# Kernel tuning notes

Measured on AMD Instinct MI355X. Metric: run time of the kernel, lower is better.

The kernel has to match this reference:

```python
import jax, jax.numpy as jnp
import numpy as np

D_MODEL = 768
N_HEADS = 12
D_K = D_MODEL // N_HEADS
EPS = 1e-5


def layer_norm(x, g, b):
    mu = jnp.mean(x, axis=-1, keepdims=True)
    var = jnp.var(x, axis=-1, keepdims=True)
    return (x - mu) * jax.lax.rsqrt(var + EPS) * g + b


def setup_inputs() -> dict:
    key = jax.random.key(0)
    ks = jax.random.split(key, 16)
    d, h = D_MODEL, 4 * D_MODEL
    s = 1.0 / np.sqrt(d)
    inp = {
        "x": jax.random.normal(ks[0], (2, 4096, d), jnp.float32),
        "wq": jax.random.normal(ks[1], (d, d), jnp.float32) * s,
        "bq": jnp.zeros((d,), jnp.float32),
        "wk": jax.random.normal(ks[2], (d, d), jnp.float32) * s,
        "bk": jnp.zeros((d,), jnp.float32),
        "wv": jax.random.normal(ks[3], (d, d), jnp.float32) * s,
        "bv": jnp.zeros((d,), jnp.float32),
        "wo": jax.random.normal(ks[4], (d, d), jnp.float32) * s,
        "bo": jnp.zeros((d,), jnp.float32),
        "w1": jax.random.normal(ks[5], (h, d), jnp.float32) * s,
        "b1": jnp.zeros((h,), jnp.float32),
        "w2": jax.random.normal(ks[6], (d, h), jnp.float32) * (1.0 / np.sqrt(h)),
        "b2": jnp.zeros((d,), jnp.float32),
        "g1": jnp.ones((d,), jnp.float32),
        "beta1": jnp.zeros((d,), jnp.float32),
        "g2": jnp.ones((d,), jnp.float32),
        "beta2": jnp.zeros((d,), jnp.float32),
    }
    return inp


def reference(x, wq, bq, wk, bk, wv, bv, wo, bo, w1, b1, w2, b2, g1, beta1, g2, beta2):
    B, S, D = x.shape
    # --- MHA (self-attention, torch Linear: y = x @ W.T + b) ---
    def heads(t):  # [B,S,D] -> [B,H,S,d_k]
        return t.reshape(B, S, N_HEADS, D_K).transpose(0, 2, 1, 3)
    q = heads(x @ wq.T + bq)
    k = heads(x @ wk.T + bk)
    v = heads(x @ wv.T + bv)
    scores = jnp.einsum("bhqd,bhkd->bhqk", q, k) / np.sqrt(D_K)
    attn = jax.nn.softmax(scores, axis=-1)
    ctx = jnp.einsum("bhqk,bhkd->bhqd", attn, v)
    ctx = ctx.transpose(0, 2, 1, 3).reshape(B, S, D)
    mha_out = ctx @ wo.T + bo
    # --- residual + LN1 ---
    n1 = layer_norm(x + mha_out, g1, beta1)
    # --- FFN (exact GELU, dropout=0/eval) ---
    hdn = jax.nn.gelu(n1 @ w1.T + b1, approximate=False)
    ffn_out = hdn @ w2.T + b2
    # --- residual + LN2 ---
    return layer_norm(n1 + ffn_out, g2, beta2)
```

## Files before the change

kernel.cpp:

```cpp
#include <hip/hip_runtime.h>
#include <cstdint>
#include <cstddef>


#define D_MODEL 768
#define N_HEADS 12
#define D_K     64
#define SEQ     4096
#define BATCH   2
#define M_ROWS  (BATCH * SEQ)
#define H_FF    3072
#define LDQKV   2304

#define QSCALE 0.18033688011112042f

typedef __bf16 bf16_t;
typedef __attribute__((ext_vector_type(8))) __bf16 bf16x8;
typedef __attribute__((ext_vector_type(4))) __bf16 bf16x4;
typedef __attribute__((ext_vector_type(2))) __bf16 bf16x2;
typedef __attribute__((ext_vector_type(4))) float  floatx4;
typedef __attribute__((ext_vector_type(4))) short  short4_t;

union bf16x4_cast { bf16x4 h; short4_t s; };

__device__ __forceinline__ float gelu_exact(float x) {
    return 0.5f * x * (1.0f + erff(x * 0.70710678118654752f));
}

#if __has_builtin(__builtin_amdgcn_exp2f)
#define EXP2F(x) __builtin_amdgcn_exp2f(x)
#else
static __device__ __forceinline__ float EXP2F(float x) {
    float r; asm("v_exp_f32 %0, %1" : "=v"(r) : "v"(x)); return r;
}
#endif

#define GLL16(gp, lp)                                                         \
    __builtin_amdgcn_global_load_lds(                                         \
        (const __attribute__((address_space(1))) void*)(gp),                  \
        (__attribute__((address_space(3))) void*)(lp), 16, 0, 0)

#define NX_V  (6291456 / 4)
#define NW_V  (589824 / 4)
#define NF_V  (2359296 / 4)
#define NCONV_V (NX_V + 4 * NW_V + 2 * NF_V)

__global__ __launch_bounds__(256) void fused_convert_kernel(
    const float* __restrict__ x,  const float* __restrict__ wq,
    const float* __restrict__ wk, const float* __restrict__ wv,
    const float* __restrict__ wo, const float* __restrict__ w1,
    const float* __restrict__ w2,
    bf16_t* __restrict__ xb, bf16_t* __restrict__ wqkvb,
    bf16_t* __restrict__ wob, bf16_t* __restrict__ w1b,
    bf16_t* __restrict__ w2b) {
    const int v = blockIdx.x * 256 + threadIdx.x;
    const float* src; bf16_t* dst; int off; float scale = 1.0f;
    if (v < NX_V)                    { src = x;  dst = xb;              off = v; }
    else if (v < NX_V + NW_V)        { src = wq; dst = wqkvb;           off = v - NX_V; scale = QSCALE; }
    else if (v < NX_V + 2 * NW_V)    { src = wk; dst = wqkvb + 589824;  off = v - NX_V - NW_V; }
    else if (v < NX_V + 3 * NW_V)    { src = wv; dst = wqkvb + 1179648; off = v - NX_V - 2 * NW_V; }
    else if (v < NX_V + 4 * NW_V)    { src = wo; dst = wob;             off = v - NX_V - 3 * NW_V; }
    else if (v < NX_V + 4 * NW_V + NF_V) { src = w1; dst = w1b;         off = v - NX_V - 4 * NW_V; }
    else                             { src = w2; dst = w2b;             off = v - NX_V - 4 * NW_V - NF_V; }
    floatx4 f = *(const floatx4*)&src[(size_t)off * 4];
    bf16x4 o = bf16x4{(bf16_t)(f[0] * scale), (bf16_t)(f[1] * scale),
                      (bf16_t)(f[2] * scale), (bf16_t)(f[3] * scale)};
    *(bf16x4*)&dst[(size_t)off * 4] = o;
}

__global__ __launch_bounds__(256) void pack_bias_kernel(
    const float* __restrict__ bq, const float* __restrict__ bk,
    const float* __restrict__ bv, float* __restrict__ dst) {
    int i = blockIdx.x * 256 + threadIdx.x;
    if (i < 768)       dst[i] = bq[i] * QSCALE;
    else if (i < 1536) dst[i] = bk[i - 768];
    else if (i < 2304) dst[i] = bv[i - 1536];
}

template<int BN>
__global__ __launch_bounds__(256) void gemm_lds_kernel(
    const bf16_t* __restrict__ A, const bf16_t* __restrict__ W,
    const float* __restrict__ bias, bf16_t* __restrict__ C,
    int M, int N, int K, int act) {

    __shared__ bf16_t As[128 * 64];
    __shared__ bf16_t Bs[BN * 64];

    const int t    = threadIdx.x;
    const int lane = t & 63;
    const int w    = t >> 6;
    const int lrow = lane & 15;
    const int quad = lane >> 4;
    const int n0   = blockIdx.x * BN;
    const int m0   = blockIdx.y * 128;

    constexpr int MI = (BN == 128) ? 4 : 2;
    constexpr int NB = (BN == 128) ? 4 : 2;
    const int wmo = (BN == 128) ? (w >> 1) * 64 : w * 32;
    const int wno = (BN == 128) ? (w & 1) * 64 : 0;

    const int srow = lane >> 3;
    const int scol = ((lane & 7) ^ srow) * 8;
    size_t a_g[4];
#pragma unroll
    for (int i = 0; i < 4; ++i)
        a_g[i] = (size_t)(m0 + (w * 4 + i) * 8 + srow) * K + scol;
    size_t b_g[NB];
#pragma unroll
    for (int i = 0; i < NB; ++i)
        b_g[i] = (size_t)(n0 + (w * NB + i) * 8 + srow) * K + scol;

    const int slot0 = (quad ^ (lrow & 7)) * 8;
    const int slot1 = slot0 ^ 32;

    floatx4 acc[MI][4];
#pragma unroll
    for (int i = 0; i < MI; ++i)
#pragma unroll
        for (int j = 0; j < 4; ++j) acc[i][j] = floatx4{0.f, 0.f, 0.f, 0.f};

    for (int k0 = 0; k0 < K; k0 += 64) {
#pragma unroll
        for (int i = 0; i < 4; ++i)
            GLL16(&A[a_g[i] + k0], &As[(w * 4 + i) * 512]);
#pragma unroll
        for (int i = 0; i < NB; ++i)
            GLL16(&W[b_g[i] + k0], &Bs[(w * NB + i) * 512]);
        __syncthreads();

#pragma unroll
        for (int kk = 0; kk < 2; ++kk) {
            const int off = kk ? slot1 : slot0;
            bf16x8 a[MI], b[4];
#pragma unroll
            for (int i = 0; i < MI; ++i)
                a[i] = *(bf16x8*)&As[(wmo + i * 16 + lrow) * 64 + off];
#pragma unroll
            for (int j = 0; j < 4; ++j)
                b[j] = *(bf16x8*)&Bs[(wno + j * 16 + lrow) * 64 + off];
#pragma unroll
            for (int i = 0; i < MI; ++i)
#pragma unroll
                for (int j = 0; j < 4; ++j)
                    acc[i][j] = __builtin_amdgcn_mfma_f32_16x16x32_bf16(
                        b[j], a[i], acc[i][j], 0, 0, 0);
        }
        __syncthreads();
    }

#pragma unroll
    for (int i = 0; i < MI; ++i) {
        const int m = m0 + wmo + i * 16 + lrow;
#pragma unroll
        for (int j = 0; j < 4; ++j) {
            const int n = n0 + wno + j * 16 + quad * 4;
            const floatx4 bv = *(const floatx4*)&bias[n];
            float v0 = acc[i][j][0] + bv[0];
            float v1 = acc[i][j][1] + bv[1];
            float v2 = acc[i][j][2] + bv[2];
            float v3 = acc[i][j][3] + bv[3];
            if (act) {
                v0 = gelu_exact(v0); v1 = gelu_exact(v1);
                v2 = gelu_exact(v2); v3 = gelu_exact(v3);
            }
            *(bf16x4*)&C[(size_t)m * N + n] =
                bf16x4{(bf16_t)v0, (bf16_t)v1, (bf16_t)v2, (bf16_t)v3};
        }
    }
}

__global__ __launch_bounds__(256, 3) void attn_kernel(
    const bf16_t* __restrict__ QKV, bf16_t* __restrict__ Ctx) {

    __shared__ bf16_t Ks[64 * 72];
    __shared__ bf16_t Vt[64 * 72];

    const int t    = threadIdx.x;
    const int lane = t & 63;
    const int w    = t >> 6;
    const int lrow = lane & 15;
    const int quad = lane >> 4;

    const int b  = blockIdx.y / N_HEADS;
    const int h  = blockIdx.y % N_HEADS;
    const int q0 = blockIdx.x * 128 + w * 32;
    const size_t base_q = ((size_t)b * SEQ) * LDQKV + h * D_K;
    const size_t base_k = base_q + 768;
    const size_t base_v = base_q + 1536;
    const size_t base_o = ((size_t)b * SEQ) * D_MODEL + h * D_K;

    bf16x8 qf[2][2];
#pragma unroll
    for (int s = 0; s < 2; ++s) {
        const size_t qrow = base_q + (size_t)(q0 + s * 16 + lrow) * LDQKV + quad * 8;
        qf[s][0] = *(const bf16x8*)&QKV[qrow];
        qf[s][1] = *(const bf16x8*)&QKV[qrow + 32];
    }

    float l_part[2] = {0.f, 0.f};
    floatx4 o_acc[2][4];
#pragma unroll
    for (int s = 0; s < 2; ++s)
#pragma unroll
        for (int d = 0; d < 4; ++d) o_acc[s][d] = floatx4{0.f, 0.f, 0.f, 0.f};

    const int skey = t >> 2;
    const int sch  = t & 3;
    const int kp   = t >> 3;
    const int sch8 = t & 7;
    const int vcol = ((2 * kp) & 63) ^ (sch8 << 3);

    const size_t gk0 = base_k + (size_t)skey * LDQKV + sch * 8;
    const size_t gv0 = base_v + (size_t)(2 * kp) * LDQKV + sch8 * 8;
    bf16x8 kv0 = *(const bf16x8*)&QKV[gk0];
    bf16x8 kv1 = *(const bf16x8*)&QKV[gk0 + 32];
    bf16x8 vv0 = *(const bf16x8*)&QKV[gv0];
    bf16x8 vv1 = *(const bf16x8*)&QKV[gv0 + LDQKV];

    for (int k0 = 0; k0 < SEQ; k0 += 64) {
        *(bf16x8*)&Ks[skey * 72 + sch * 8]      = kv0;
        *(bf16x8*)&Ks[skey * 72 + sch * 8 + 32] = kv1;
#pragma unroll
        for (int j = 0; j < 8; ++j)
            *(bf16x2*)&Vt[(sch8 * 8 + j) * 72 + vcol] = bf16x2{vv0[j], vv1[j]};
        __syncthreads();

        if (k0 + 64 < SEQ) {
            const size_t gk = gk0 + (size_t)(k0 + 64) * LDQKV;
            const size_t gv = gv0 + (size_t)(k0 + 64) * LDQKV;
            kv0 = *(const bf16x8*)&QKV[gk];
            kv1 = *(const bf16x8*)&QKV[gk + 32];
            vv0 = *(const bf16x8*)&QKV[gv];
            vv1 = *(const bf16x8*)&QKV[gv + LDQKV];
        }

        __builtin_amdgcn_s_setprio(1);
        short4_t p[2][4];
#pragma unroll
        for (int kt = 0; kt < 4; ++kt) {
            bf16x8 ka0 = *(bf16x8*)&Ks[(kt * 16 + lrow) * 72 + quad * 8];
            bf16x8 ka1 = *(bf16x8*)&Ks[(kt * 16 + lrow) * 72 + 32 + quad * 8];
            floatx4 z = floatx4{0.f, 0.f, 0.f, 0.f};
#pragma unroll
            for (int s = 0; s < 2; ++s) {
                floatx4 st = __builtin_amdgcn_mfma_f32_16x16x32_bf16(ka0, qf[s][0], z, 0, 0, 0);
                st = __builtin_amdgcn_mfma_f32_16x16x32_bf16(ka1, qf[s][1], st, 0, 0, 0);
                float p0 = EXP2F(st[0]), p1 = EXP2F(st[1]);
                float p2 = EXP2F(st[2]), p3 = EXP2F(st[3]);
                l_part[s] += (p0 + p1) + (p2 + p3);
                bf16x4_cast pc;
                pc.h = bf16x4{(bf16_t)p0, (bf16_t)p1, (bf16_t)p2, (bf16_t)p3};
                p[s][kt] = pc.s;
            }
        }

#pragma unroll
        for (int dt = 0; dt < 4; ++dt) {
            const int d   = dt * 16 + lrow;
            const int swv = ((d >> 3) & 7) << 3;
#pragma unroll
            for (int kc = 0; kc < 4; ++kc) {
                bf16x4_cast ac;
                ac.h = *(bf16x4*)&Vt[d * 72 + ((kc * 16 + quad * 4) ^ swv)];
                o_acc[0][dt] = __builtin_amdgcn_mfma_f32_16x16x16bf16_1k(
                    ac.s, p[0][kc], o_acc[0][dt], 0, 0, 0);
                o_acc[1][dt] = __builtin_amdgcn_mfma_f32_16x16x16bf16_1k(
                    ac.s, p[1][kc], o_acc[1][dt], 0, 0, 0);
            }
        }
        __builtin_amdgcn_s_setprio(0);
        __syncthreads();
    }

#pragma unroll
    for (int s = 0; s < 2; ++s) {
        float lsum = l_part[s];
        lsum += __shfl_xor(lsum, 16, 64);
        lsum += __shfl_xor(lsum, 32, 64);
        const float inv = 1.0f / lsum;
        const size_t orow = base_o + (size_t)(q0 + s * 16 + lrow) * D_MODEL;
#pragma unroll
        for (int dt = 0; dt < 4; ++dt) {
            bf16x4 ov = bf16x4{(bf16_t)(o_acc[s][dt][0] * inv),
                               (bf16_t)(o_acc[s][dt][1] * inv),
                               (bf16_t)(o_acc[s][dt][2] * inv),
                               (bf16_t)(o_acc[s][dt][3] * inv)};
            *(bf16x4*)&Ctx[orow + dt * 16 + quad * 4] = ov;
        }
    }
}

__global__ __launch_bounds__(256) void ln_res_f32in_kernel(
    const float* __restrict__ x, const bf16_t* __restrict__ res,
    const float* __restrict__ g, const float* __restrict__ be,
    bf16_t* __restrict__ out) {
    const int row = blockIdx.x, t = threadIdx.x;
    const size_t base = (size_t)row * D_MODEL;
    float vals[3], sum = 0.f, sq = 0.f;
#pragma unroll
    for (int it = 0; it < 3; ++it) {
        int i = t + it * 256;
        float v = x[base + i] + (float)res[base + i];
        vals[it] = v; sum += v; sq += v * v;
    }
#pragma unroll
    for (int d = 1; d < 64; d <<= 1) { sum += __shfl_xor(sum, d, 64); sq += __shfl_xor(sq, d, 64); }
    __shared__ float ssum[4], ssq[4], s_mu, s_rs;
    if ((t & 63) == 0) { ssum[t >> 6] = sum; ssq[t >> 6] = sq; }
    __syncthreads();
    if (t == 0) {
        float S = ssum[0] + ssum[1] + ssum[2] + ssum[3];
        float Qq = ssq[0] + ssq[1] + ssq[2] + ssq[3];
        float mu = S / D_MODEL;
        s_mu = mu;
        s_rs = rsqrtf(Qq / D_MODEL - mu * mu + 1e-5f);
    }
    __syncthreads();
    const float mu = s_mu, rs = s_rs;
#pragma unroll
    for (int it = 0; it < 3; ++it) {
        int i = t + it * 256;
        out[base + i] = (bf16_t)((vals[it] - mu) * rs * g[i] + be[i]);
    }
}

__global__ __launch_bounds__(256) void ln_res_final_kernel(
    const bf16_t* __restrict__ a, const bf16_t* __restrict__ bfb,
    const float* __restrict__ g, const float* __restrict__ be,
    float* __restrict__ out) {
    const int row = blockIdx.x, t = threadIdx.x;
    const size_t base = (size_t)row * D_MODEL;
    float vals[3], sum = 0.f, sq = 0.f;
#pragma unroll
    for (int it = 0; it < 3; ++it) {
        int i = t + it * 256;
        float v = (float)a[base + i] + (float)bfb[base + i];
        vals[it] = v; sum += v; sq += v * v;
    }
#pragma unroll
    for (int d = 1; d < 64; d <<= 1) { sum += __shfl_xor(sum, d, 64); sq += __shfl_xor(sq, d, 64); }
    __shared__ float ssum[4], ssq[4], s_mu, s_rs;
    if ((t & 63) == 0) { ssum[t >> 6] = sum; ssq[t >> 6] = sq; }
    __syncthreads();
    if (t == 0) {
        float S = ssum[0] + ssum[1] + ssum[2] + ssum[3];
        float Qq = ssq[0] + ssq[1] + ssq[2] + ssq[3];
        float mu = S / D_MODEL;
        s_mu = mu;
        s_rs = rsqrtf(Qq / D_MODEL - mu * mu + 1e-5f);
    }
    __syncthreads();
    const float mu = s_mu, rs = s_rs;
#pragma unroll
    for (int it = 0; it < 3; ++it) {
        int i = t + it * 256;
        out[base + i] = (vals[it] - mu) * rs * g[i] + be[i];
    }
}

extern "C" void kernel_launch(void* const* d_in, const int* in_sizes, int n_in,
                              void* d_out, int out_size, void* d_ws, size_t ws_size,
                              hipStream_t stream) {
    const float* x    = (const float*)d_in[0];
    const float* wq   = (const float*)d_in[1];
    const float* bq   = (const float*)d_in[2];
    const float* wk   = (const float*)d_in[3];
    const float* bk   = (const float*)d_in[4];
    const float* wv   = (const float*)d_in[5];
    const float* bv   = (const float*)d_in[6];
    const float* wo   = (const float*)d_in[7];
    const float* bo   = (const float*)d_in[8];
    const float* w1   = (const float*)d_in[9];
    const float* b1   = (const float*)d_in[10];
    const float* w2   = (const float*)d_in[11];
    const float* b2   = (const float*)d_in[12];
    const float* g1   = (const float*)d_in[13];
    const float* be1  = (const float*)d_in[14];
    const float* g2   = (const float*)d_in[15];
    const float* be2  = (const float*)d_in[16];
    float* out = (float*)d_out;

    char* ws = (char*)d_ws;
    const size_t SZ_XB   = (size_t)M_ROWS * D_MODEL * 2;
    const size_t SZ_QKV  = (size_t)M_ROWS * LDQKV * 2;
    const size_t SZ_CTX  = SZ_XB;
    const size_t SZ_H    = (size_t)M_ROWS * H_FF * 2;
    const size_t SZ_WQKV = (size_t)LDQKV * D_MODEL * 2;
    const size_t SZ_WO   = (size_t)D_MODEL * D_MODEL * 2;
    const size_t SZ_W1   = (size_t)H_FF * D_MODEL * 2;

    bf16_t* xb    = (bf16_t*)(ws);
    bf16_t* qkvb  = (bf16_t*)(ws + SZ_XB);
    bf16_t* ctxb  = (bf16_t*)(ws + SZ_XB + SZ_QKV);
    bf16_t* hb    = (bf16_t*)(ws + SZ_XB + SZ_QKV + SZ_CTX);
    char*   wsw   = ws + SZ_XB + SZ_QKV + SZ_CTX + SZ_H;
    bf16_t* wqkvb = (bf16_t*)(wsw);
    bf16_t* wob   = (bf16_t*)(wsw + SZ_WQKV);
    bf16_t* w1b   = (bf16_t*)(wsw + SZ_WQKV + SZ_WO);
    bf16_t* w2b   = (bf16_t*)(wsw + SZ_WQKV + SZ_WO + SZ_W1);
    float*  bqkv  = (float*)(wsw + SZ_WQKV + SZ_WO + 2 * SZ_W1);
    bf16_t* mhab  = qkvb;
    bf16_t* n1b   = xb;
    bf16_t* ffb   = ctxb;

    fused_convert_kernel<<<NCONV_V / 256, 256, 0, stream>>>(
        x, wq, wk, wv, wo, w1, w2, xb, wqkvb, wob, w1b, w2b);
    pack_bias_kernel<<<9, 256, 0, stream>>>(bq, bk, bv, bqkv);

    gemm_lds_kernel<128><<<dim3(LDQKV / 128, M_ROWS / 128), 256, 0, stream>>>(
        xb, wqkvb, bqkv, qkvb, M_ROWS, LDQKV, D_MODEL, 0);

    attn_kernel<<<dim3(SEQ / 128, BATCH * N_HEADS), 256, 0, stream>>>(qkvb, ctxb);

    gemm_lds_kernel<64><<<dim3(D_MODEL / 64, M_ROWS / 128), 256, 0, stream>>>(
        ctxb, wob, bo, mhab, M_ROWS, D_MODEL, D_MODEL, 0);

    ln_res_f32in_kernel<<<M_ROWS, 256, 0, stream>>>(x, mhab, g1, be1, n1b);

    gemm_lds_kernel<128><<<dim3(H_FF / 128, M_ROWS / 128), 256, 0, stream>>>(
        n1b, w1b, b1, hb, M_ROWS, H_FF, D_MODEL, 1);

    gemm_lds_kernel<64><<<dim3(D_MODEL / 64, M_ROWS / 128), 256, 0, stream>>>(
        hb, w2b, b2, ffb, M_ROWS, D_MODEL, H_FF, 0);

    ln_res_final_kernel<<<M_ROWS, 256, 0, stream>>>(n1b, ffb, g2, be2, out);
}
```

Baseline: 483.0 us.

## Split-K the FFN down-projection and fold partial sums into final LayerNorm

Replaces the W2 GEMM (K=3072, N=768, 64-wide tiles) with a 128x128-tile split-K kernel whose two halves write fp32 partials into the output buffer and the reused QKV buffer. The final residual LayerNorm kernel now sums both partials and adds the bias itself. The aim is larger tiles with better data reuse while keeping enough blocks in flight, and no bf16 rounding of the FFN output. In exchange, the fp32 partials add extra global memory writes and reads.

```diff
diff --git a/kernel.cpp b/kernel.cpp
--- a/kernel.cpp
+++ b/kernel.cpp
@@ -169,6 +169,85 @@
     }
 }
 
+__global__ __launch_bounds__(256) void gemm_splitk_kernel(
+    const bf16_t* __restrict__ A, const bf16_t* __restrict__ W,
+    float* __restrict__ P0, float* __restrict__ P1,
+    int M, int N, int K) {
+
+    __shared__ bf16_t As[128 * 64];
+    __shared__ bf16_t Bs[128 * 64];
+
+    const int t    = threadIdx.x;
+    const int lane = t & 63;
+    const int w    = t >> 6;
+    const int lrow = lane & 15;
+    const int quad = lane >> 4;
+    const int n0   = blockIdx.x * 128;
+    const int m0   = blockIdx.y * 128;
+    const int kb   = blockIdx.z * (K / 2);
+
+    const int wmo = (w >> 1) * 64;
+    const int wno = (w & 1) * 64;
+
+    const int srow = lane >> 3;
+    const int scol = ((lane & 7) ^ srow) * 8;
+    size_t a_g[4], b_g[4];
+#pragma unroll
+    for (int i = 0; i < 4; ++i) {
+        a_g[i] = (size_t)(m0 + (w * 4 + i) * 8 + srow) * K + kb + scol;
+        b_g[i] = (size_t)(n0 + (w * 4 + i) * 8 + srow) * K + kb + scol;
+    }
+
+    const int slot0 = (quad ^ (lrow & 7)) * 8;
+    const int slot1 = slot0 ^ 32;
+
+    floatx4 acc[4][4];
+#pragma unroll
+    for (int i = 0; i < 4; ++i)
+#pragma unroll
+        for (int j = 0; j < 4; ++j) acc[i][j] = floatx4{0.f, 0.f, 0.f, 0.f};
+
+    for (int k0 = 0; k0 < K / 2; k0 += 64) {
+#pragma unroll
+        for (int i = 0; i < 4; ++i)
+            GLL16(&A[a_g[i] + k0], &As[(w * 4 + i) * 512]);
+#pragma unroll
+        for (int i = 0; i < 4; ++i)
+            GLL16(&W[b_g[i] + k0], &Bs[(w * 4 + i) * 512]);
+        __syncthreads();
+
+#pragma unroll
+        for (int kk = 0; kk < 2; ++kk) {
+            const int off = kk ? slot1 : slot0;
+            bf16x8 a[4], b[4];
+#pragma unroll
+            for (int i = 0; i < 4; ++i)
+                a[i] = *(bf16x8*)&As[(wmo + i * 16 + lrow) * 64 + off];
+#pragma unroll
+            for (int j = 0; j < 4; ++j)
+                b[j] = *(bf16x8*)&Bs[(wno + j * 16 + lrow) * 64 + off];
+#pragma unroll
+            for (int i = 0; i < 4; ++i)
+#pragma unroll
+                for (int j = 0; j < 4; ++j)
+                    acc[i][j] = __builtin_amdgcn_mfma_f32_16x16x32_bf16(
+                        b[j], a[i], acc[i][j], 0, 0, 0);
+        }
+        __syncthreads();
+    }
+
+    float* __restrict__ P = blockIdx.z ? P1 : P0;
+#pragma unroll
+    for (int i = 0; i < 4; ++i) {
+        const int m = m0 + wmo + i * 16 + lrow;
+#pragma unroll
+        for (int j = 0; j < 4; ++j) {
+            const int n = n0 + wno + j * 16 + quad * 4;
+            *(floatx4*)&P[(size_t)m * N + n] = acc[i][j];
+        }
+    }
+}
+
 __global__ __launch_bounds__(256, 3) void attn_kernel(
     const bf16_t* __restrict__ QKV, bf16_t* __restrict__ Ctx) {
 
@@ -325,7 +404,8 @@
 }
 
 __global__ __launch_bounds__(256) void ln_res_final_kernel(
-    const bf16_t* __restrict__ a, const bf16_t* __restrict__ bfb,
+    const bf16_t* __restrict__ a, const float* __restrict__ p0,
+    const float* __restrict__ p1, const float* __restrict__ b2,
     const float* __restrict__ g, const float* __restrict__ be,
     float* __restrict__ out) {
     const int row = blockIdx.x, t = threadIdx.x;
@@ -334,7 +414,7 @@
 #pragma unroll
     for (int it = 0; it < 3; ++it) {
         int i = t + it * 256;
-        float v = (float)a[base + i] + (float)bfb[base + i];
+        float v = (float)a[base + i] + p0[base + i] + p1[base + i] + b2[i];
         vals[it] = v; sum += v; sq += v * v;
     }
 #pragma unroll
@@ -401,7 +481,8 @@
     float*  bqkv  = (float*)(wsw + SZ_WQKV + SZ_WO + 2 * SZ_W1);
     bf16_t* mhab  = qkvb;
     bf16_t* n1b   = xb;
-    bf16_t* ffb   = ctxb;
+    float*  p0    = out;
+    float*  p1    = (float*)qkvb;
 
     fused_convert_kernel<<<NCONV_V / 256, 256, 0, stream>>>(
         x, wq, wk, wv, wo, w1, w2, xb, wqkvb, wob, w1b, w2b);
@@ -420,8 +501,8 @@
     gemm_lds_kernel<128><<<dim3(H_FF / 128, M_ROWS / 128), 256, 0, stream>>>(
         n1b, w1b, b1, hb, M_ROWS, H_FF, D_MODEL, 1);
 
-    gemm_lds_kernel<64><<<dim3(D_MODEL / 64, M_ROWS / 128), 256, 0, stream>>>(
-        hb, w2b, b2, ffb, M_ROWS, D_MODEL, H_FF, 0);
-
-    ln_res_final_kernel<<<M_ROWS, 256, 0, stream>>>(n1b, ffb, g2, be2, out);
-}
+    gemm_splitk_kernel<<<dim3(D_MODEL / 128, M_ROWS / 128, 2), 256, 0, stream>>>(
+        hb, w2b, p0, p1, M_ROWS, D_MODEL, H_FF);
+
+    ln_res_final_kernel<<<M_ROWS, 256, 0, stream>>>(n1b, p0, p1, b2, g2, be2, out);
+}
```

Result: no change. 486.9 us (+0.8%).

## Double-buffer K/V shared tiles in attention kernel to drop one barrier per tile

Applied to the files above, without the earlier changes.

Attention now keeps two shared-memory buffers for the K and transposed V tiles. Each iteration computes on the current buffer, then writes the already-prefetched next tile into the other buffer and issues global loads two tiles ahead. This removes one __syncthreads per key tile and lets the LDS writes overlap with other waves' compute. In exchange it doubles LDS use (about 36KB per block), which may lower occupancy under the 3-blocks-per-SM launch bound, and the register-prefetched global loads must now complete before the store at the end of the same iteration.

```diff
diff --git a/kernel.cpp b/kernel.cpp
--- a/kernel.cpp
+++ b/kernel.cpp
@@ -172,8 +172,8 @@
 __global__ __launch_bounds__(256, 3) void attn_kernel(
     const bf16_t* __restrict__ QKV, bf16_t* __restrict__ Ctx) {
 
-    __shared__ bf16_t Ks[64 * 72];
-    __shared__ bf16_t Vt[64 * 72];
+    __shared__ bf16_t Ks[2][64 * 72];
+    __shared__ bf16_t Vt[2][64 * 72];
 
     const int t    = threadIdx.x;
     const int lane = t & 63;
@@ -212,34 +212,37 @@
 
     const size_t gk0 = base_k + (size_t)skey * LDQKV + sch * 8;
     const size_t gv0 = base_v + (size_t)(2 * kp) * LDQKV + sch8 * 8;
+
     bf16x8 kv0 = *(const bf16x8*)&QKV[gk0];
     bf16x8 kv1 = *(const bf16x8*)&QKV[gk0 + 32];
     bf16x8 vv0 = *(const bf16x8*)&QKV[gv0];
     bf16x8 vv1 = *(const bf16x8*)&QKV[gv0 + LDQKV];
-
+    *(bf16x8*)&Ks[0][skey * 72 + sch * 8]      = kv0;
+    *(bf16x8*)&Ks[0][skey * 72 + sch * 8 + 32] = kv1;
+#pragma unroll
+    for (int j = 0; j < 8; ++j)
+        *(bf16x2*)&Vt[0][(sch8 * 8 + j) * 72 + vcol] = bf16x2{vv0[j], vv1[j]};
+    {
+        const size_t gk = gk0 + (size_t)64 * LDQKV;
+        const size_t gv = gv0 + (size_t)64 * LDQKV;
+        kv0 = *(const bf16x8*)&QKV[gk];
+        kv1 = *(const bf16x8*)&QKV[gk + 32];
+        vv0 = *(const bf16x8*)&QKV[gv];
+        vv1 = *(const bf16x8*)&QKV[gv + LDQKV];
+    }
+    __syncthreads();
+
+    int cur = 0;
     for (int k0 = 0; k0 < SEQ; k0 += 64) {
-        *(bf16x8*)&Ks[skey * 72 + sch * 8]      = kv0;
-        *(bf16x8*)&Ks[skey * 72 + sch * 8 + 32] = kv1;
-#pragma unroll
-        for (int j = 0; j < 8; ++j)
-            *(bf16x2*)&Vt[(sch8 * 8 + j) * 72 + vcol] = bf16x2{vv0[j], vv1[j]};
-        __syncthreads();
-
-        if (k0 + 64 < SEQ) {
-            const size_t gk = gk0 + (size_t)(k0 + 64) * LDQKV;
-            const size_t gv = gv0 + (size_t)(k0 + 64) * LDQKV;
-            kv0 = *(const bf16x8*)&QKV[gk];
-            kv1 = *(const bf16x8*)&QKV[gk + 32];
-            vv0 = *(const bf16x8*)&QKV[gv];
-            vv1 = *(const bf16x8*)&QKV[gv + LDQKV];
-        }
+        const bf16_t* ks = Ks[cur];
+        const bf16_t* vt = Vt[cur];
 
         __builtin_amdgcn_s_setprio(1);
         short4_t p[2][4];
 #pragma unroll
         for (int kt = 0; kt < 4; ++kt) {
-            bf16x8 ka0 = *(bf16x8*)&Ks[(kt * 16 + lrow) * 72 + quad * 8];
-            bf16x8 ka1 = *(bf16x8*)&Ks[(kt * 16 + lrow) * 72 + 32 + quad * 8];
+            bf16x8 ka0 = *(bf16x8*)&ks[(kt * 16 + lrow) * 72 + quad * 8];
+            bf16x8 ka1 = *(bf16x8*)&ks[(kt * 16 + lrow) * 72 + 32 + quad * 8];
             floatx4 z = floatx4{0.f, 0.f, 0.f, 0.f};
 #pragma unroll
             for (int s = 0; s < 2; ++s) {
@@ -261,7 +264,7 @@
 #pragma unroll
             for (int kc = 0; kc < 4; ++kc) {
                 bf16x4_cast ac;
-                ac.h = *(bf16x4*)&Vt[d * 72 + ((kc * 16 + quad * 4) ^ swv)];
+                ac.h = *(bf16x4*)&vt[d * 72 + ((kc * 16 + quad * 4) ^ swv)];
                 o_acc[0][dt] = __builtin_amdgcn_mfma_f32_16x16x16bf16_1k(
                     ac.s, p[0][kc], o_acc[0][dt], 0, 0, 0);
                 o_acc[1][dt] = __builtin_amdgcn_mfma_f32_16x16x16bf16_1k(
@@ -269,7 +272,26 @@
             }
         }
         __builtin_amdgcn_s_setprio(0);
+
+        if (k0 + 64 < SEQ) {
+            bf16_t* ksn = Ks[cur ^ 1];
+            bf16_t* vtn = Vt[cur ^ 1];
+            *(bf16x8*)&ksn[skey * 72 + sch * 8]      = kv0;
+            *(bf16x8*)&ksn[skey * 72 + sch * 8 + 32] = kv1;
+#pragma unroll
+            for (int j = 0; j < 8; ++j)
+                *(bf16x2*)&vtn[(sch8 * 8 + j) * 72 + vcol] = bf16x2{vv0[j], vv1[j]};
+            if (k0 + 128 < SEQ) {
+                const size_t gk = gk0 + (size_t)(k0 + 128) * LDQKV;
+                const size_t gv = gv0 + (size_t)(k0 + 128) * LDQKV;
+                kv0 = *(const bf16x8*)&QKV[gk];
+                kv1 = *(const bf16x8*)&QKV[gk + 32];
+                vv0 = *(const bf16x8*)&QKV[gv];
+                vv1 = *(const bf16x8*)&QKV[gv + LDQKV];
+            }
+        }
         __syncthreads();
+        cur ^= 1;
     }
 
 #pragma unroll
```

Result: no change. 490.8 us (+1.6%).

## Double-buffer K/V shared memory tiles in attention kernel

Applied to the files above, without the earlier changes.

Splits the K and V shared-memory tiles into two buffers and unrolls the key loop by two. While one tile is being computed, the next tile is written to the other buffer, so there is one barrier per tile instead of two. This is meant to overlap LDS writes and global prefetch with the MFMA work and cut synchronisation stalls. The cost is double the LDS footprint and extra registers for two prefetched tiles, which could reduce occupancy.

```diff
diff --git a/kernel.cpp b/kernel.cpp
--- a/kernel.cpp
+++ b/kernel.cpp
@@ -172,8 +172,8 @@
 __global__ __launch_bounds__(256, 3) void attn_kernel(
     const bf16_t* __restrict__ QKV, bf16_t* __restrict__ Ctx) {
 
-    __shared__ bf16_t Ks[64 * 72];
-    __shared__ bf16_t Vt[64 * 72];
+    __shared__ bf16_t Ks[2][64 * 72];
+    __shared__ bf16_t Vt[2][64 * 72];
 
     const int t    = threadIdx.x;
     const int lane = t & 63;
@@ -212,63 +212,84 @@
 
     const size_t gk0 = base_k + (size_t)skey * LDQKV + sch * 8;
     const size_t gv0 = base_v + (size_t)(2 * kp) * LDQKV + sch8 * 8;
-    bf16x8 kv0 = *(const bf16x8*)&QKV[gk0];
-    bf16x8 kv1 = *(const bf16x8*)&QKV[gk0 + 32];
-    bf16x8 vv0 = *(const bf16x8*)&QKV[gv0];
-    bf16x8 vv1 = *(const bf16x8*)&QKV[gv0 + LDQKV];
-
-    for (int k0 = 0; k0 < SEQ; k0 += 64) {
-        *(bf16x8*)&Ks[skey * 72 + sch * 8]      = kv0;
-        *(bf16x8*)&Ks[skey * 72 + sch * 8 + 32] = kv1;
-#pragma unroll
-        for (int j = 0; j < 8; ++j)
-            *(bf16x2*)&Vt[(sch8 * 8 + j) * 72 + vcol] = bf16x2{vv0[j], vv1[j]};
+
+#define ATTN_LOAD(koff, KV0, KV1, VV0, VV1)                                   \
+    {                                                                         \
+        const size_t gk_ = gk0 + (size_t)(koff) * LDQKV;                      \
+        const size_t gv_ = gv0 + (size_t)(koff) * LDQKV;                      \
+        KV0 = *(const bf16x8*)&QKV[gk_];                                      \
+        KV1 = *(const bf16x8*)&QKV[gk_ + 32];                                 \
+        VV0 = *(const bf16x8*)&QKV[gv_];                                      \
+        VV1 = *(const bf16x8*)&QKV[gv_ + LDQKV];                              \
+    }
+
+#define ATTN_WRITE(BUF, KV0, KV1, VV0, VV1)                                   \
+    {                                                                         \
+        bf16_t* ksn_ = Ks[BUF];                                               \
+        bf16_t* vtn_ = Vt[BUF];                                               \
+        *(bf16x8*)&ksn_[skey * 72 + sch * 8]      = KV0;                      \
+        *(bf16x8*)&ksn_[skey * 72 + sch * 8 + 32] = KV1;                      \
+        _Pragma("unroll")                                                     \
+        for (int j = 0; j < 8; ++j)                                           \
+            *(bf16x2*)&vtn_[(sch8 * 8 + j) * 72 + vcol] = bf16x2{VV0[j], VV1[j]}; \
+    }
+
+#define ATTN_COMPUTE(CUR)                                                     \
+    {                                                                         \
+        const bf16_t* ks_ = Ks[CUR];                                          \
+        const bf16_t* vt_ = Vt[CUR];                                          \
+        __builtin_amdgcn_s_setprio(1);                                        \
+        short4_t p[2][4];                                                     \
+        _Pragma("unroll")                                                     \
+        for (int kt = 0; kt < 4; ++kt) {                                      \
+            bf16x8 ka0 = *(bf16x8*)&ks_[(kt * 16 + lrow) * 72 + quad * 8];    \
+            bf16x8 ka1 = *(bf16x8*)&ks_[(kt * 16 + lrow) * 72 + 32 + quad * 8]; \
+            floatx4 z = floatx4{0.f, 0.f, 0.f, 0.f};                          \
+            _Pragma("unroll")                                                 \
+            for (int s = 0; s < 2; ++s) {                                     \
+                floatx4 st = __builtin_amdgcn_mfma_f32_16x16x32_bf16(ka0, qf[s][0], z, 0, 0, 0); \
+                st = __builtin_amdgcn_mfma_f32_16x16x32_bf16(ka1, qf[s][1], st, 0, 0, 0); \
+                float p0 = EXP2F(st[0]), p1 = EXP2F(st[1]);                   \
+                float p2 = EXP2F(st[2]), p3 = EXP2F(st[3]);                   \
+                l_part[s] += (p0 + p1) + (p2 + p3);                           \
+                bf16x4_cast pc;                                               \
+                pc.h = bf16x4{(bf16_t)p0, (bf16_t)p1, (bf16_t)p2, (bf16_t)p3}; \
+                p[s][kt] = pc.s;                                              \
+            }                                                                 \
+        }                                                                     \
+        _Pragma("unroll")                                                     \
+        for (int dt = 0; dt < 4; ++dt) {                                      \
+            const int d_  = dt * 16 + lrow;                                   \
+            const int swv = ((d_ >> 3) & 7) << 3;                             \
+            _Pragma("unroll")                                                 \
+            for (int kc = 0; kc < 4; ++kc) {                                  \
+                bf16x4_cast ac;                                               \
+                ac.h = *(bf16x4*)&vt_[d_ * 72 + ((kc * 16 + quad * 4) ^ swv)]; \
+                o_acc[0][dt] = __builtin_amdgcn_mfma_f32_16x16x16bf16_1k(     \
+                    ac.s, p[0][kc], o_acc[0][dt], 0, 0, 0);                   \
+                o_acc[1][dt] = __builtin_amdgcn_mfma_f32_16x16x16bf16_1k(     \
+                    ac.s, p[1][kc], o_acc[1][dt], 0, 0, 0);                   \
+            }                                                                 \
+        }                                                                     \
+        __builtin_amdgcn_s_setprio(0);                                        \
+    }
+
+    bf16x8 akv0, akv1, avv0, avv1;
+    bf16x8 bkv0, bkv1, bvv0, bvv1;
+
+    ATTN_LOAD(0, akv0, akv1, avv0, avv1);
+    ATTN_WRITE(0, akv0, akv1, avv0, avv1);
+    ATTN_LOAD(64, bkv0, bkv1, bvv0, bvv1);
+    __syncthreads();
+
+    for (int k0 = 0; k0 < SEQ; k0 += 128) {
+        if (k0 + 128 < SEQ) ATTN_LOAD(k0 + 128, akv0, akv1, avv0, avv1);
+        ATTN_COMPUTE(0);
+        ATTN_WRITE(1, bkv0, bkv1, bvv0, bvv1);
         __syncthreads();
-
-        if (k0 + 64 < SEQ) {
-            const size_t gk = gk0 + (size_t)(k0 + 64) * LDQKV;
-            const size_t gv = gv0 + (size_t)(k0 + 64) * LDQKV;
-            kv0 = *(const bf16x8*)&QKV[gk];
-            kv1 = *(const bf16x8*)&QKV[gk + 32];
-            vv0 = *(const bf16x8*)&QKV[gv];
-            vv1 = *(const bf16x8*)&QKV[gv + LDQKV];
-        }
-
-        __builtin_amdgcn_s_setprio(1);
-        short4_t p[2][4];
-#pragma unroll
-        for (int kt = 0; kt < 4; ++kt) {
-            bf16x8 ka0 = *(bf16x8*)&Ks[(kt * 16 + lrow) * 72 + quad * 8];
-            bf16x8 ka1 = *(bf16x8*)&Ks[(kt * 16 + lrow) * 72 + 32 + quad * 8];
-            floatx4 z = floatx4{0.f, 0.f, 0.f, 0.f};
-#pragma unroll
-            for (int s = 0; s < 2; ++s) {
-                floatx4 st = __builtin_amdgcn_mfma_f32_16x16x32_bf16(ka0, qf[s][0], z, 0, 0, 0);
-                st = __builtin_amdgcn_mfma_f32_16x16x32_bf16(ka1, qf[s][1], st, 0, 0, 0);
-                float p0 = EXP2F(st[0]), p1 = EXP2F(st[1]);
-                float p2 = EXP2F(st[2]), p3 = EXP2F(st[3]);
-                l_part[s] += (p0 + p1) + (p2 + p3);
-                bf16x4_cast pc;
-                pc.h = bf16x4{(bf16_t)p0, (bf16_t)p1, (bf16_t)p2, (bf16_t)p3};
-                p[s][kt] = pc.s;
-            }
-        }
-
-#pragma unroll
-        for (int dt = 0; dt < 4; ++dt) {
-            const int d   = dt * 16 + lrow;
-            const int swv = ((d >> 3) & 7) << 3;
-#pragma unroll
-            for (int kc = 0; kc < 4; ++kc) {
-                bf16x4_cast ac;
-                ac.h = *(bf16x4*)&Vt[d * 72 + ((kc * 16 + quad * 4) ^ swv)];
-                o_acc[0][dt] = __builtin_amdgcn_mfma_f32_16x16x16bf16_1k(
-                    ac.s, p[0][kc], o_acc[0][dt], 0, 0, 0);
-                o_acc[1][dt] = __builtin_amdgcn_mfma_f32_16x16x16bf16_1k(
-                    ac.s, p[1][kc], o_acc[1][dt], 0, 0, 0);
-            }
-        }
-        __builtin_amdgcn_s_setprio(0);
+        if (k0 + 192 < SEQ) ATTN_LOAD(k0 + 192, bkv0, bkv1, bvv0, bvv1);
+        ATTN_COMPUTE(1);
+        if (k0 + 128 < SEQ) ATTN_WRITE(0, akv0, akv1, avv0, avv1);
         __syncthreads();
     }
 
```

Measured after the change: 609.8 us. 26.3% more time.
